# Performance work log

Measured on AMD Instinct MI355X. Metric: run time of the kernel, lower is better.

The kernel has to match this reference:

```python
import jax, jax.numpy as jnp
import numpy as np

B = 262144       # batch_size
N = 64           # n_nodes in the DAG
K = 4            # max parents per node (banded DAG: parents i-K..i-1)
NH = 10          # hidden width of each CGNN_block


def setup_inputs() -> dict:
    key = jax.random.key(0)
    k_noise, k_w1, k_b1, k_w2, k_b2 = jax.random.split(key, 5)
    # DAG structure: node i's parents are max(0, i-K)..i-1, padded with -1.
    pidx = -np.ones((N, K), dtype=np.int32)
    for i in range(N):
        ps = list(range(max(0, i - K), i))
        pidx[i, :len(ps)] = ps
    noise = jax.random.normal(k_noise, (B, N), dtype=jnp.float32)
    # Per-node MLP params, padded to max input width K+1. Padded parent slots
    # feed zeros, so extra weight rows never contribute.
    W1 = jax.random.normal(k_w1, (N, K + 1, NH), dtype=jnp.float32) * 0.3
    b1 = jax.random.normal(k_b1, (N, NH), dtype=jnp.float32) * 0.1
    W2 = jax.random.normal(k_w2, (N, NH), dtype=jnp.float32) * 0.3
    b2 = jax.random.normal(k_b2, (N,), dtype=jnp.float32) * 0.1
    return {"noise": noise, "parent_idx": jnp.asarray(pidx),
            "W1": W1, "b1": b1, "W2": W2, "b2": b2}


def reference(noise, parent_idx, W1, b1, W2, b2):
    n_nodes = parent_idx.shape[0]

    def step(gen, xs):
        # gen: [B, N] generated values so far (topological order = 0..N-1)
        pidx, W1i, b1i, W2i, b2i, ncol, i = xs
        mask = (pidx >= 0).astype(gen.dtype)                # [K]
        vals = gen[:, jnp.clip(pidx, 0, None)] * mask       # [B, K]
        x = jnp.concatenate([vals, ncol[:, None]], axis=1)  # [B, K+1]
        h = jax.nn.relu(x @ W1i + b1i)                      # [B, NH]
        y = h @ W2i + b2i                                   # [B]
        return gen.at[:, i].set(y), None

    gen0 = jnp.zeros_like(noise)
    xs = (parent_idx, W1, b1, W2, b2, noise.T, jnp.arange(n_nodes))
    gen, _ = jax.lax.scan(step, gen0, xs)
    return gen  # torch.cat(self.generated, 1) -> [B, N]
```

## Files before the change

### kernel.cpp

```cpp
#include <hip/hip_runtime.h>


#define NN   64
#define KP   4
#define NHID 10
#define BLK  256
#define W1N  ((KP + 1) * NHID)

__device__ __forceinline__ float cgnn_node(
    const float* __restrict__ w1,
    const float* __restrict__ b1n,
    const float* __restrict__ w2,
    const float* __restrict__ b2n,
    float p0, float p1, float p2, float p3, float nv)
{
    float h[NHID];
#pragma unroll
    for (int j = 0; j < NHID; ++j) h[j] = b1n[j];
#pragma unroll
    for (int j = 0; j < NHID; ++j) h[j] = fmaf(p0, w1[0 * NHID + j], h[j]);
#pragma unroll
    for (int j = 0; j < NHID; ++j) h[j] = fmaf(p1, w1[1 * NHID + j], h[j]);
#pragma unroll
    for (int j = 0; j < NHID; ++j) h[j] = fmaf(p2, w1[2 * NHID + j], h[j]);
#pragma unroll
    for (int j = 0; j < NHID; ++j) h[j] = fmaf(p3, w1[3 * NHID + j], h[j]);
#pragma unroll
    for (int j = 0; j < NHID; ++j) h[j] = fmaf(nv, w1[4 * NHID + j], h[j]);

    float p[NHID];
#pragma unroll
    for (int j = 0; j < NHID; ++j) p[j] = fmaxf(h[j], 0.0f) * w2[j];
    const float t01 = p[0] + p[1], t23 = p[2] + p[3];
    const float t45 = p[4] + p[5], t67 = p[6] + p[7];
    return b2n[0] + ((t01 + t23) + (t45 + t67)) + (p[8] + p[9]);
}

__global__ __launch_bounds__(256) void cgnn_fwd(
    const float* __restrict__ noise,
    const float* __restrict__ W1,
    const float* __restrict__ b1,
    const float* __restrict__ W2,
    const float* __restrict__ b2,
    float* __restrict__ out,
    int B)
{
    __shared__ float4 smem[4 * 64 * 8];

    const int tid  = threadIdx.x;
    const int wave = tid >> 6;
    const int lane = tid & 63;

    const float4* __restrict__ gnoise = reinterpret_cast<const float4*>(noise);
    float4* __restrict__ gout = reinterpret_cast<float4*>(out);
    const size_t waveRow0 = (size_t)blockIdx.x * BLK + wave * 64;

    float4* const wbuf = &smem[wave * 512];

    float c0 = 0.f, c1 = 0.f, c2 = 0.f, c3 = 0.f;

#pragma unroll 1
    for (int half = 0; half < 2; ++half) {
#pragma unroll 1
        for (int k = 0; k < 8; ++k) {
            const int idx = k * 64 + lane;
            const int r = idx >> 3, c4 = idx & 7;
            wbuf[r * 8 + (c4 ^ (r & 7))] =
                gnoise[(waveRow0 + r) * (NN / 4) + half * 8 + c4];
        }

#pragma unroll 1
        for (int qq = 0; qq < 8; ++qq) {
            const int q = half * 8 + qq;
            const float4 nz = wbuf[lane * 8 + (qq ^ (lane & 7))];

            const float* w1q = W1 + q * 4 * W1N;
            const float* b1q = b1 + q * 4 * NHID;
            const float* w2q = W2 + q * 4 * NHID;
            const float* b2q = b2 + q * 4;

            float n0, n1, n2, n3;
            if (q == 0) {
                n0 = cgnn_node(w1q,            b1q,            w2q,            b2q,     0.f, 0.f, 0.f, 0.f, nz.x);
                n1 = cgnn_node(w1q + W1N,      b1q + NHID,     w2q + NHID,     b2q + 1, n0,  0.f, 0.f, 0.f, nz.y);
                n2 = cgnn_node(w1q + 2 * W1N,  b1q + 2 * NHID, w2q + 2 * NHID, b2q + 2, n0,  n1,  0.f, 0.f, nz.z);
                n3 = cgnn_node(w1q + 3 * W1N,  b1q + 3 * NHID, w2q + 3 * NHID, b2q + 3, n0,  n1,  n2,  0.f, nz.w);
            } else {
                n0 = cgnn_node(w1q,            b1q,            w2q,            b2q,     c0, c1, c2, c3, nz.x);
                n1 = cgnn_node(w1q + W1N,      b1q + NHID,     w2q + NHID,     b2q + 1, c1, c2, c3, n0, nz.y);
                n2 = cgnn_node(w1q + 2 * W1N,  b1q + 2 * NHID, w2q + 2 * NHID, b2q + 2, c2, c3, n0, n1, nz.z);
                n3 = cgnn_node(w1q + 3 * W1N,  b1q + 3 * NHID, w2q + 3 * NHID, b2q + 3, c3, n0, n1, n2, nz.w);
            }

            wbuf[lane * 8 + (qq ^ (lane & 7))] = make_float4(n0, n1, n2, n3);
            c0 = n0; c1 = n1; c2 = n2; c3 = n3;
        }

#pragma unroll 1
        for (int k = 0; k < 8; ++k) {
            const int idx = k * 64 + lane;
            const int r = idx >> 3, c4 = idx & 7;
            gout[(waveRow0 + r) * (NN / 4) + half * 8 + c4] =
                wbuf[r * 8 + (c4 ^ (r & 7))];
        }
    }
}

extern "C" void kernel_launch(void* const* d_in, const int* in_sizes, int n_in,
                              void* d_out, int out_size, void* d_ws, size_t ws_size,
                              hipStream_t stream) {
    const float* noise = (const float*)d_in[0];
    const float* W1 = (const float*)d_in[2];
    const float* b1 = (const float*)d_in[3];
    const float* W2 = (const float*)d_in[4];
    const float* b2 = (const float*)d_in[5];
    float* out = (float*)d_out;

    const int B = in_sizes[0] / NN;
    const int blocks = B / BLK;
    cgnn_fwd<<<blocks, BLK, 0, stream>>>(noise, W1, b1, W2, b2, out, B);
}
```

Before: 169.7 us.

## Stage packed per-node weights in LDS and shrink noise staging to quarters

Each block first copies all 64 nodes' MLP parameters into LDS, packed at 72 floats per node, and reads them as float4 broadcasts instead of scalar global/constant loads. The noise/output staging buffer is cut from 8 to 4 float4 columns per row, processed in four quarters. This is meant to remove scalar-cache and global weight-fetch latency from the serial node chain. In exchange every block pays a prologue that loads about 18 KB of weights plus a barrier, uses more LDS, and the 72-float weight array per node may raise register pressure.

```diff
diff --git a/kernel.cpp b/kernel.cpp
--- a/kernel.cpp
+++ b/kernel.cpp
@@ -5,36 +5,8 @@
 #define KP   4
 #define NHID 10
 #define BLK  256
-#define W1N  ((KP + 1) * NHID)
-
-__device__ __forceinline__ float cgnn_node(
-    const float* __restrict__ w1,
-    const float* __restrict__ b1n,
-    const float* __restrict__ w2,
-    const float* __restrict__ b2n,
-    float p0, float p1, float p2, float p3, float nv)
-{
-    float h[NHID];
-#pragma unroll
-    for (int j = 0; j < NHID; ++j) h[j] = b1n[j];
-#pragma unroll
-    for (int j = 0; j < NHID; ++j) h[j] = fmaf(p0, w1[0 * NHID + j], h[j]);
-#pragma unroll
-    for (int j = 0; j < NHID; ++j) h[j] = fmaf(p1, w1[1 * NHID + j], h[j]);
-#pragma unroll
-    for (int j = 0; j < NHID; ++j) h[j] = fmaf(p2, w1[2 * NHID + j], h[j]);
-#pragma unroll
-    for (int j = 0; j < NHID; ++j) h[j] = fmaf(p3, w1[3 * NHID + j], h[j]);
-#pragma unroll
-    for (int j = 0; j < NHID; ++j) h[j] = fmaf(nv, w1[4 * NHID + j], h[j]);
-
-    float p[NHID];
-#pragma unroll
-    for (int j = 0; j < NHID; ++j) p[j] = fmaxf(h[j], 0.0f) * w2[j];
-    const float t01 = p[0] + p[1], t23 = p[2] + p[3];
-    const float t45 = p[4] + p[5], t67 = p[6] + p[7];
-    return b2n[0] + ((t01 + t23) + (t45 + t67)) + (p[8] + p[9]);
-}
+#define NODE_F 72
+#define WTOT (NN * NODE_F)
 
 __global__ __launch_bounds__(256) void cgnn_fwd(
     const float* __restrict__ noise,
@@ -45,63 +17,106 @@
     float* __restrict__ out,
     int B)
 {
-    __shared__ float4 smem[4 * 64 * 8];
+    __shared__ float  wlds[WTOT];
+    __shared__ float4 stage[4 * 64 * 4];
 
     const int tid  = threadIdx.x;
     const int wave = tid >> 6;
     const int lane = tid & 63;
 
+#pragma unroll 1
+    for (int k = 0; k < WTOT / BLK; ++k) {
+        const int idx  = k * BLK + tid;
+        const int node = idx / NODE_F;
+        const int o    = idx - node * NODE_F;
+        float v;
+        if      (o < 10) v = b1[node * NHID + o];
+        else if (o < 60) v = W1[node * (KP + 1) * NHID + (o - 10)];
+        else if (o < 70) v = W2[node * NHID + (o - 60)];
+        else if (o == 70) v = b2[node];
+        else              v = 0.0f;
+        wlds[idx] = v;
+    }
+    __syncthreads();
+
     const float4* __restrict__ gnoise = reinterpret_cast<const float4*>(noise);
     float4* __restrict__ gout = reinterpret_cast<float4*>(out);
     const size_t waveRow0 = (size_t)blockIdx.x * BLK + wave * 64;
 
-    float4* const wbuf = &smem[wave * 512];
+    float4* const wbuf = &stage[wave * 256];
+
+    auto node_eval = [&](int i, float p0, float p1, float p2, float p3,
+                         float nv) -> float {
+        const float4* __restrict__ p4 =
+            reinterpret_cast<const float4*>(&wlds[i * NODE_F]);
+        float wv[NODE_F];
+#pragma unroll
+        for (int c = 0; c < NODE_F / 4; ++c) {
+            const float4 v = p4[c];
+            wv[4 * c + 0] = v.x; wv[4 * c + 1] = v.y;
+            wv[4 * c + 2] = v.z; wv[4 * c + 3] = v.w;
+        }
+        float h[NHID];
+#pragma unroll
+        for (int j = 0; j < NHID; ++j) h[j] = wv[j];
+#pragma unroll
+        for (int j = 0; j < NHID; ++j) h[j] = fmaf(p0, wv[10 + j], h[j]);
+#pragma unroll
+        for (int j = 0; j < NHID; ++j) h[j] = fmaf(p1, wv[20 + j], h[j]);
+#pragma unroll
+        for (int j = 0; j < NHID; ++j) h[j] = fmaf(p2, wv[30 + j], h[j]);
+#pragma unroll
+        for (int j = 0; j < NHID; ++j) h[j] = fmaf(p3, wv[40 + j], h[j]);
+#pragma unroll
+        for (int j = 0; j < NHID; ++j) h[j] = fmaf(nv, wv[50 + j], h[j]);
+        float p[NHID];
+#pragma unroll
+        for (int j = 0; j < NHID; ++j) p[j] = fmaxf(h[j], 0.0f) * wv[60 + j];
+        const float t01 = p[0] + p[1], t23 = p[2] + p[3];
+        const float t45 = p[4] + p[5], t67 = p[6] + p[7];
+        return wv[70] + ((t01 + t23) + (t45 + t67)) + (p[8] + p[9]);
+    };
 
     float c0 = 0.f, c1 = 0.f, c2 = 0.f, c3 = 0.f;
 
 #pragma unroll 1
-    for (int half = 0; half < 2; ++half) {
+    for (int quarter = 0; quarter < 4; ++quarter) {
 #pragma unroll 1
-        for (int k = 0; k < 8; ++k) {
+        for (int k = 0; k < 4; ++k) {
             const int idx = k * 64 + lane;
-            const int r = idx >> 3, c4 = idx & 7;
-            wbuf[r * 8 + (c4 ^ (r & 7))] =
-                gnoise[(waveRow0 + r) * (NN / 4) + half * 8 + c4];
+            const int r = idx >> 2, c4 = idx & 3;
+            wbuf[r * 4 + (c4 ^ (r & 3))] =
+                gnoise[(waveRow0 + r) * (NN / 4) + quarter * 4 + c4];
         }
 
 #pragma unroll 1
-        for (int qq = 0; qq < 8; ++qq) {
-            const int q = half * 8 + qq;
-            const float4 nz = wbuf[lane * 8 + (qq ^ (lane & 7))];
-
-            const float* w1q = W1 + q * 4 * W1N;
-            const float* b1q = b1 + q * 4 * NHID;
-            const float* w2q = W2 + q * 4 * NHID;
-            const float* b2q = b2 + q * 4;
+        for (int qq = 0; qq < 4; ++qq) {
+            const int q = quarter * 4 + qq;
+            const float4 nz = wbuf[lane * 4 + (qq ^ (lane & 3))];
 
             float n0, n1, n2, n3;
             if (q == 0) {
-                n0 = cgnn_node(w1q,            b1q,            w2q,            b2q,     0.f, 0.f, 0.f, 0.f, nz.x);
-                n1 = cgnn_node(w1q + W1N,      b1q + NHID,     w2q + NHID,     b2q + 1, n0,  0.f, 0.f, 0.f, nz.y);
-                n2 = cgnn_node(w1q + 2 * W1N,  b1q + 2 * NHID, w2q + 2 * NHID, b2q + 2, n0,  n1,  0.f, 0.f, nz.z);
-                n3 = cgnn_node(w1q + 3 * W1N,  b1q + 3 * NHID, w2q + 3 * NHID, b2q + 3, n0,  n1,  n2,  0.f, nz.w);
+                n0 = node_eval(0, 0.f, 0.f, 0.f, 0.f, nz.x);
+                n1 = node_eval(1, n0,  0.f, 0.f, 0.f, nz.y);
+                n2 = node_eval(2, n0,  n1,  0.f, 0.f, nz.z);
+                n3 = node_eval(3, n0,  n1,  n2,  0.f, nz.w);
             } else {
-                n0 = cgnn_node(w1q,            b1q,            w2q,            b2q,     c0, c1, c2, c3, nz.x);
-                n1 = cgnn_node(w1q + W1N,      b1q + NHID,     w2q + NHID,     b2q + 1, c1, c2, c3, n0, nz.y);
-                n2 = cgnn_node(w1q + 2 * W1N,  b1q + 2 * NHID, w2q + 2 * NHID, b2q + 2, c2, c3, n0, n1, nz.z);
-                n3 = cgnn_node(w1q + 3 * W1N,  b1q + 3 * NHID, w2q + 3 * NHID, b2q + 3, c3, n0, n1, n2, nz.w);
+                n0 = node_eval(q * 4 + 0, c0, c1, c2, c3, nz.x);
+                n1 = node_eval(q * 4 + 1, c1, c2, c3, n0, nz.y);
+                n2 = node_eval(q * 4 + 2, c2, c3, n0, n1, nz.z);
+                n3 = node_eval(q * 4 + 3, c3, n0, n1, n2, nz.w);
             }
 
-            wbuf[lane * 8 + (qq ^ (lane & 7))] = make_float4(n0, n1, n2, n3);
+            wbuf[lane * 4 + (qq ^ (lane & 3))] = make_float4(n0, n1, n2, n3);
             c0 = n0; c1 = n1; c2 = n2; c3 = n3;
         }
 
 #pragma unroll 1
-        for (int k = 0; k < 8; ++k) {
+        for (int k = 0; k < 4; ++k) {
             const int idx = k * 64 + lane;
-            const int r = idx >> 3, c4 = idx & 7;
-            gout[(waveRow0 + r) * (NN / 4) + half * 8 + c4] =
-                wbuf[r * 8 + (c4 ^ (r & 7))];
+            const int r = idx >> 2, c4 = idx & 3;
+            gout[(waveRow0 + r) * (NN / 4) + quarter * 4 + c4] =
+                wbuf[r * 4 + (c4 ^ (r & 3))];
         }
     }
 }
```

Measured after the change: 220.4 us. 29.9% more time.
